# Kernel optimization log

Hardware: AMD Instinct MI355X
Metric: run time of the kernel (lower is better)

The kernel has to match this reference:

```python
import jax, jax.numpy as jnp
import numpy as np

B, N, F_IN = 2048, 64, 49   # batch of molecules, max atoms, atom feature size
D, H, L = 256, 8, 6         # conv_dim, num_heads, n_GAT_layer
DK = D // H                 # per-head dim
FC = 128                    # fc_dim
ALPHA = 0.2                 # LeakyReLU slope in GAT
NEG_INF = -1e9


def setup_inputs() -> dict:
    key = jax.random.key(0)
    ks = jax.random.split(key, 10)
    # --- padded molecular graphs ---
    n_atoms = jax.random.randint(ks[0], (B,), 16, N + 1)
    valid = jnp.arange(N)[None, :] < n_atoms[:, None]                  # [B,N]
    r = jax.random.uniform(ks[1], (B, N, N))
    adj = ((r + jnp.swapaxes(r, 1, 2)) * 0.5) < 0.08                   # symmetric sparse bonds
    adj = adj | jnp.eye(N, dtype=bool)[None]                           # self loops
    adj = adj & valid[:, :, None] & valid[:, None, :]                  # zero padded atoms
    A = adj.astype(jnp.float32)                                        # [B,N,N]
    x = jax.random.normal(ks[2], (B, N, F_IN), dtype=jnp.float32)      # [B,N,49]
    # --- parameters (xavier-like scaling) ---
    W_emb = jax.random.normal(ks[3], (D, F_IN), dtype=jnp.float32) * 0.08
    gat_W = jax.random.normal(ks[4], (L, D, D), dtype=jnp.float32) * 0.06
    gat_b = jnp.zeros((L, D), dtype=jnp.float32)
    gat_a = jax.random.normal(ks[5], (L, H, 2 * DK), dtype=jnp.float32) * 0.1
    fc_W1 = jax.random.normal(ks[6], (FC, D), dtype=jnp.float32) * 0.07
    fc_b1 = jnp.zeros((FC,), dtype=jnp.float32)
    fc_W2 = jax.random.normal(ks[7], (FC, FC), dtype=jnp.float32) * 0.09
    fc_b2 = jnp.zeros((FC,), dtype=jnp.float32)
    fc_W3 = jax.random.normal(ks[8], (1, FC), dtype=jnp.float32) * 0.09
    fc_b3 = jnp.zeros((1,), dtype=jnp.float32)
    return dict(x=x, A=A, W_emb=W_emb, gat_W=gat_W, gat_b=gat_b, gat_a=gat_a,
                fc_W1=fc_W1, fc_b1=fc_b1, fc_W2=fc_W2, fc_b2=fc_b2,
                fc_W3=fc_W3, fc_b3=fc_b3)


def _gat_layer(x, A, W, b, a):
    # x: [B,N,D], A: [B,N,N], W: [D,D], b: [D], a: [H,2*DK]
    Bm, Nn, Dd = x.shape
    h = (x @ W.T + b).reshape(Bm, Nn, H, DK)                           # [B,N,H,DK]
    a_src, a_dst = a[:, :DK], a[:, DK:]                                # [H,DK]
    e_src = jnp.einsum('bnhd,hd->bnh', h, a_src)                       # [B,N,H]
    e_dst = jnp.einsum('bnhd,hd->bnh', h, a_dst)
    e = jax.nn.leaky_relu(e_src[:, :, None, :] + e_dst[:, None, :, :], ALPHA)  # [B,Ni,Nj,H]
    e = jnp.where((A > 0)[..., None], e, NEG_INF)                      # adjacency mask
    attn = jax.nn.softmax(e, axis=2)                                   # softmax over neighbors j
    out = jnp.einsum('bijh,bjhd->bihd', attn, h).reshape(Bm, Nn, Dd)
    return jax.nn.elu(out + x)                                         # residual + ELU


def reference(x, A, W_emb, gat_W, gat_b, gat_a,
              fc_W1, fc_b1, fc_W2, fc_b2, fc_W3, fc_b3):
    h = x @ W_emb.T                                                    # embedding (no bias)
    for l in range(L):                                                 # dropout p=0 -> identity
        h = _gat_layer(h, A, gat_W[l], gat_b[l], gat_a[l])
    # masked mean readout
    node_mask = (A.sum(-1) > 0).astype(h.dtype)                        # [B,N]
    w = node_mask / node_mask.sum(-1, keepdims=True)
    g = (h * w[..., None]).sum(1)                                      # [B,D]
    # dense head: 256 -> 128 -> 128 -> 1
    z = jax.nn.relu(g @ fc_W1.T + fc_b1)
    z = jax.nn.relu(z @ fc_W2.T + fc_b2)
    z = z @ fc_W3.T + fc_b3                                            # [B,1]
    return jax.nn.elu(z).squeeze(-1) + 1.5                             # [B]
```

## Files before the change

### kernel.cpp

```cpp
#include <hip/hip_runtime.h>
#include <cstdint>
#include <cstddef>

#define B_GRAPHS 2048
#define N_NODES  64
#define FIN      49
#define D_DIM    256
#define H_HEADS  8
#define DK_DIM   32
#define L_LAYERS 6
#define ALPHA    0.2f
#define LOG2E    1.4426950408889634f

#define M_FULL     (B_GRAPHS * N_NODES)
#define WSLAB      (256 * 256)

typedef __bf16 bf16x8 __attribute__((ext_vector_type(8)));
typedef __bf16 bf16x4 __attribute__((ext_vector_type(4)));
typedef float  f32x4  __attribute__((ext_vector_type(4)));

#define MFMA16(a, b, c) __builtin_amdgcn_mfma_f32_16x16x32_bf16(a, b, c, 0, 0, 0)

__device__ __forceinline__ float leaky(float t) { return t > 0.f ? t : ALPHA * t; }

#define LDS_H     0
#define LDS_V     32768
#define LDS_E     49152
#define LDS_AM    53248
#define LDS_VALID 53760
#define LDS_TOTAL 53776

__global__ void convert_weights(const float* __restrict__ W_emb,
                                const float* __restrict__ gat_W,
                                const float* __restrict__ gat_a,
                                const float* __restrict__ gat_b,
                                __bf16* __restrict__ Wemb_b,
                                __bf16* __restrict__ Wb,
                                float* __restrict__ ba)
{
    int idx = blockIdx.x * 256 + threadIdx.x;
    if (idx < 256 * 64) {
        int n = idx >> 6, k = idx & 63;
        float f = (k < FIN) ? W_emb[n * FIN + k] : 0.f;
        Wemb_b[idx] = (__bf16)f;
    }
    if (idx < L_LAYERS * 65536) {
        Wb[idx] = (__bf16)gat_W[idx];
    }
    int o2 = idx - L_LAYERS * 65536;
    if (o2 >= 0 && o2 < L_LAYERS * 16) {
        int l = o2 >> 4, c = o2 & 15;
        int hh = c >> 1, sd = c & 1;
        const float* av = gat_a + l * 512 + hh * 64 + sd * 32;
        const float* bp = gat_b + l * 256 + hh * 32;
        float s = 0.f;
        for (int d = 0; d < 32; d++) s += av[d] * bp[d];
        ba[o2] = s;
    }
}

__global__ void convert_x(const float* __restrict__ x, __bf16* __restrict__ xb)
{
    int idx = blockIdx.x * 256 + threadIdx.x;
    int m = idx >> 6, k = idx & 63;
    xb[idx] = (__bf16)((k < FIN) ? x[m * FIN + k] : 0.f);
}

__global__ __launch_bounds__(256, 2)
void mega_gat(const float* __restrict__ A,
              const __bf16* __restrict__ xb,
              const __bf16* __restrict__ Wemb,
              const __bf16* __restrict__ Wb_all,
              const float* __restrict__ gat_b_all,
              const float* __restrict__ a_all,
              const float* __restrict__ ba_all,
              const float* __restrict__ W1, const float* __restrict__ b1,
              const float* __restrict__ W2, const float* __restrict__ b2,
              const float* __restrict__ W3, const float* __restrict__ b3,
              float* __restrict__ out)
{
    __shared__ __align__(16) char smem[LDS_TOTAL];

    const int tid  = threadIdx.x;
    const int lane = tid & 63;
    const int w    = tid >> 6;
    const int q    = lane >> 4;
    const int d15  = lane & 15;
    const int g    = blockIdx.x;

    char*  vwbase = smem + LDS_V + w * 4096;
    float* E      = (float*)(smem + LDS_E + w * 1024);
    unsigned long long* Am = (unsigned long long*)(smem + LDS_AM);

    auto h_off = [&](int i, int d) -> int {
        return i * 512 + ((((d >> 3) ^ (i & 7)) << 4)) + ((d & 7) << 1);
    };

    {
        const char* src = (const char*)(xb + (size_t)g * 4096);
        bf16x8 t0 = *(const bf16x8*)(src + tid * 16);
        bf16x8 t1 = *(const bf16x8*)(src + 4096 + tid * 16);
        int u0 = tid, u1 = 256 + tid;
        int r0 = u0 >> 3, s0 = u0 & 7;
        int r1 = u1 >> 3, s1 = u1 & 7;
        *(bf16x8*)(smem + LDS_V + r0 * 128 + ((s0 ^ (r0 & 7)) << 4)) = t0;
        *(bf16x8*)(smem + LDS_V + r1 * 128 + ((s1 ^ (r1 & 7)) << 4)) = t1;
    }
    {
        const float* Ab = A + (size_t)g * 4096;
#pragma unroll
        for (int rr = 0; rr < 16; rr++) {
            int r = w * 16 + rr;
            unsigned long long m = __ballot(Ab[r * 64 + lane] > 0.f);
            if (lane == 0) Am[r] = m;
        }
    }
    __syncthreads();

    if (w == 0) {
        unsigned long long rowm = Am[lane];
        unsigned long long vmw = __ballot((rowm >> lane) & 1ULL);
        if (lane == 0) {
            *(unsigned long long*)(smem + LDS_VALID) = vmw;
            *(float*)(smem + LDS_VALID + 8) = 1.f / (float)__popcll(vmw);
        }
    }

    {
        f32x4 acc[4][4];
#pragma unroll
        for (int i = 0; i < 4; i++)
#pragma unroll
            for (int j = 0; j < 4; j++) acc[i][j] = (f32x4){0.f, 0.f, 0.f, 0.f};
#pragma unroll
        for (int ks = 0; ks < 2; ks++) {
            const int k0 = ks * 32 + q * 8;
            const int sl = ks * 4 + q;
            bf16x8 ah[4];
#pragma unroll
            for (int mf = 0; mf < 4; mf++) {
                int r = mf * 16 + d15;
                ah[mf] = *(const bf16x8*)(smem + LDS_V + r * 128 + ((sl ^ (r & 7)) << 4));
            }
#pragma unroll
            for (int nf = 0; nf < 4; nf++) {
                bf16x8 bh = *(const bf16x8*)(Wemb + (size_t)(w * 64 + nf * 16 + d15) * 64 + k0);
#pragma unroll
                for (int mf = 0; mf < 4; mf++)
                    acc[mf][nf] = MFMA16(ah[mf], bh, acc[mf][nf]);
            }
        }
#pragma unroll
        for (int nf = 0; nf < 4; nf++) {
            int d = w * 64 + nf * 16 + d15;
#pragma unroll
            for (int mf = 0; mf < 4; mf++)
#pragma unroll
                for (int rr = 0; rr < 4; rr++) {
                    int i = mf * 16 + q * 4 + rr;
                    *(__bf16*)(smem + h_off(i, d)) = (__bf16)acc[mf][nf][rr];
                }
        }
    }
    __syncthreads();

    const unsigned long long vm = *(const unsigned long long*)(smem + LDS_VALID);

#pragma unroll 1
    for (int l = 0; l < L_LAYERS; l++) {
        const __bf16* Wl = Wb_all + (size_t)l * WSLAB;

        float a0r[2][2], a1r[2][2], bar[2][2], bvreg[4];
#pragma unroll
        for (int hp = 0; hp < 2; hp++) {
            const int head = 2 * w + hp;
#pragma unroll
            for (int sd = 0; sd < 2; sd++) {
                a0r[hp][sd] = a_all[l * 512 + head * 64 + sd * 32 + d15];
                a1r[hp][sd] = a_all[l * 512 + head * 64 + sd * 32 + 16 + d15];
                bar[hp][sd] = ba_all[l * 16 + 2 * head + sd];
            }
        }
#pragma unroll
        for (int nf = 0; nf < 4; nf++)
            bvreg[nf] = gat_b_all[l * 256 + w * 64 + nf * 16 + d15];

        f32x4 acc[4][4];
#pragma unroll
        for (int i = 0; i < 4; i++)
#pragma unroll
            for (int j = 0; j < 4; j++) acc[i][j] = (f32x4){0.f, 0.f, 0.f, 0.f};

        bf16x8 breg[3][4];
        auto loadB = [&](int buf, int ks) {
            const int k0 = ks * 32 + q * 8;
#pragma unroll
            for (int nf = 0; nf < 4; nf++)
                breg[buf][nf] = *(const bf16x8*)(Wl + (size_t)(w * 64 + nf * 16 + d15) * 256 + k0);
        };
        loadB(0, 0);
        loadB(1, 1);

#pragma unroll
        for (int ks = 0; ks < 8; ks++) {
            if (ks + 2 < 8) loadB((ks + 2) % 3, ks + 2);
            bf16x8 ah[4];
            const int sl = ks * 4 + q;
#pragma unroll
            for (int mf = 0; mf < 4; mf++) {
                int r = mf * 16 + d15;
                ah[mf] = *(const bf16x8*)(smem + r * 512 + ((sl ^ (r & 7)) << 4));
            }
#pragma unroll
            for (int nf = 0; nf < 4; nf++)
#pragma unroll
                for (int mf = 0; mf < 4; mf++)
                    acc[mf][nf] = MFMA16(ah[mf], breg[ks % 3][nf], acc[mf][nf]);
        }

        __syncthreads();

        unsigned long long msk[4];
#pragma unroll
        for (int mf = 0; mf < 4; mf++) msk[mf] = Am[mf * 16 + d15];

#pragma unroll
        for (int hl = 0; hl < 2; hl++) {
            const int head = 2 * w + hl;

#pragma unroll
            for (int sd = 0; sd < 2; sd++) {
                float a0 = a0r[hl][sd];
                float a1 = a1r[hl][sd];
                float tmp[4][4];
#pragma unroll
                for (int mf = 0; mf < 4; mf++)
#pragma unroll
                    for (int rr = 0; rr < 4; rr++)
                        tmp[mf][rr] = acc[mf][2 * hl][rr] * a0 + acc[mf][2 * hl + 1][rr] * a1;
#pragma unroll
                for (int off = 1; off <= 8; off <<= 1)
#pragma unroll
                    for (int mf = 0; mf < 4; mf++)
#pragma unroll
                        for (int rr = 0; rr < 4; rr++)
                            tmp[mf][rr] += __shfl_xor(tmp[mf][rr], off);
                float bac = bar[hl][sd];
                if (d15 == 0) {
#pragma unroll
                    for (int mf = 0; mf < 4; mf++)
#pragma unroll
                        for (int rr = 0; rr < 4; rr++)
                            E[(hl * 2 + sd) * 64 + mf * 16 + q * 4 + rr] =
                                (tmp[mf][rr] + bac) * LOG2E;
                }
            }

#pragma unroll
            for (int nfl = 0; nfl < 2; nfl++) {
                const int nf = hl * 2 + nfl;
                const int d  = nfl * 16 + d15;
                const float bv = bvreg[nf];
                char* vb = vwbase + d * 128;
#pragma unroll
                for (int mf = 0; mf < 4; mf++) {
                    int s   = mf * 2 + (q >> 1);
                    int off = ((s ^ (d & 7)) << 4) + (q & 1) * 8;
                    bf16x4 h4;
#pragma unroll
                    for (int rr = 0; rr < 4; rr++)
                        h4[rr] = (__bf16)(acc[mf][nf][rr] + bv);
                    *(bf16x4*)(vb + off) = h4;
                }
            }

            float ev = E[(hl * 2 + 1) * 64 + lane];
#pragma unroll
            for (int off = 32; off; off >>= 1) ev = fmaxf(ev, __shfl_xor(ev, off));

            float esi[4], mh[4];
#pragma unroll
            for (int mf = 0; mf < 4; mf++) {
                esi[mf] = E[(hl * 2) * 64 + mf * 16 + d15];
                mh[mf]  = leaky(esi[mf] + ev);
            }

            f32x4 pv[4][2];
#pragma unroll
            for (int mf = 0; mf < 4; mf++) {
                pv[mf][0] = (f32x4){0.f, 0.f, 0.f, 0.f};
                pv[mf][1] = (f32x4){0.f, 0.f, 0.f, 0.f};
            }
            float rs[4] = {0.f, 0.f, 0.f, 0.f};

#pragma unroll
            for (int ksj = 0; ksj < 2; ksj++) {
                const int j8 = ksj * 32 + q * 8;
                const int s  = ksj * 4 + q;
                bf16x8 vh[2];
#pragma unroll
                for (int nf2 = 0; nf2 < 2; nf2++) {
                    int d = nf2 * 16 + d15;
                    vh[nf2] = *(const bf16x8*)(vwbase + d * 128 + ((s ^ (d & 7)) << 4));
                }
                float edv[8];
#pragma unroll
                for (int e = 0; e < 8; e++) edv[e] = E[(hl * 2 + 1) * 64 + j8 + e];

#pragma unroll
                for (int mf = 0; mf < 4; mf++) {
                    unsigned int mb = (unsigned int)(msk[mf] >> j8) & 0xffu;
                    bf16x8 ph;
                    float rsum = 0.f;
#pragma unroll
                    for (int e = 0; e < 8; e++) {
                        float t = leaky(esi[mf] + edv[e]);
                        float p = ((mb >> e) & 1u)
                                    ? __builtin_amdgcn_exp2f(t - mh[mf]) : 0.f;
                        rsum += p;
                        ph[e] = (__bf16)p;
                    }
                    rs[mf] += rsum;
#pragma unroll
                    for (int nf2 = 0; nf2 < 2; nf2++)
                        pv[mf][nf2] = MFMA16(ph, vh[nf2], pv[mf][nf2]);
                }
            }

#pragma unroll
            for (int mf = 0; mf < 4; mf++) {
                float r = rs[mf];
                r += __shfl_xor(r, 16);
                r += __shfl_xor(r, 32);
                if (q == 0)
                    E[(hl * 2) * 64 + mf * 16 + d15] = (r > 0.f) ? 1.f / r : 0.f;
            }

#pragma unroll
            for (int mf = 0; mf < 4; mf++) {
#pragma unroll
                for (int nf2 = 0; nf2 < 2; nf2++) {
                    int d = head * 32 + nf2 * 16 + d15;
#pragma unroll
                    for (int rr = 0; rr < 4; rr++) {
                        int i = mf * 16 + q * 4 + rr;
                        float inv = E[(hl * 2) * 64 + i];
                        int hoff = h_off(i, d);
                        float old = (float)*(const __bf16*)(smem + hoff);
                        float o = pv[mf][nf2][rr] * inv + old;
                        o = o > 0.f ? o : __expf(o) - 1.f;
                        *(__bf16*)(smem + hoff) = (__bf16)o;
                    }
                }
            }
        }
        __syncthreads();
    }

    {
        float invc = *(const float*)(smem + LDS_VALID + 8);
        float gsum = 0.f;
#pragma unroll 8
        for (int n = 0; n < 64; n++)
            if ((vm >> n) & 1ULL)
                gsum += (float)*(const __bf16*)(smem + h_off(n, tid));

        float* gl = (float*)(smem + LDS_V);
        float* z1 = (float*)(smem + LDS_V + 1024);
        float* z2 = (float*)(smem + LDS_V + 1536);
        gl[tid] = gsum * invc;
        __syncthreads();

        if (tid < 128) {
            const float* wr = W1 + tid * 256;
            float z = 0.f;
#pragma unroll 8
            for (int k = 0; k < 256; k += 4) {
                float4 wv = *(const float4*)&wr[k];
                z += wv.x * gl[k] + wv.y * gl[k + 1] + wv.z * gl[k + 2] + wv.w * gl[k + 3];
            }
            z += b1[tid];
            z1[tid] = z > 0.f ? z : 0.f;
        }
        __syncthreads();

        if (tid < 128) {
            const float* wr = W2 + tid * 128;
            float z = 0.f;
#pragma unroll 8
            for (int k = 0; k < 128; k += 4) {
                float4 wv = *(const float4*)&wr[k];
                z += wv.x * z1[k] + wv.y * z1[k + 1] + wv.z * z1[k + 2] + wv.w * z1[k + 3];
            }
            z += b2[tid];
            z2[tid] = z > 0.f ? z : 0.f;
        }
        __syncthreads();

        if (tid < 64) {
            float p = W3[tid] * z2[tid] + W3[tid + 64] * z2[tid + 64];
#pragma unroll
            for (int off = 32; off; off >>= 1) p += __shfl_down(p, off);
            if (tid == 0) {
                float z = p + b3[0];
                out[g] = (z > 0.f ? z : __expf(z) - 1.f) + 1.5f;
            }
        }
    }
}

extern "C" void kernel_launch(void* const* d_in, const int* in_sizes, int n_in,
                              void* d_out, int out_size, void* d_ws, size_t ws_size,
                              hipStream_t stream)
{
    const float* x      = (const float*)d_in[0];
    const float* A      = (const float*)d_in[1];
    const float* W_emb  = (const float*)d_in[2];
    const float* gat_W  = (const float*)d_in[3];
    const float* gat_b  = (const float*)d_in[4];
    const float* gat_a  = (const float*)d_in[5];
    const float* fc_W1  = (const float*)d_in[6];
    const float* fc_b1  = (const float*)d_in[7];
    const float* fc_W2  = (const float*)d_in[8];
    const float* fc_b2  = (const float*)d_in[9];
    const float* fc_W3  = (const float*)d_in[10];
    const float* fc_b3  = (const float*)d_in[11];
    float* out = (float*)d_out;

    char* ws = (char*)d_ws;
    __bf16* xb     = (__bf16*)ws;
    __bf16* Wemb_b = (__bf16*)(ws + 16777216);
    __bf16* Wb     = (__bf16*)(ws + 16809984);
    float*  ba     = (float*)(ws + 17596416);

    int conv_total = L_LAYERS * 65536 + L_LAYERS * 16;
    convert_weights<<<(conv_total + 255) / 256, 256, 0, stream>>>(
        W_emb, gat_W, gat_a, gat_b, Wemb_b, Wb, ba);
    convert_x<<<M_FULL * 64 / 256, 256, 0, stream>>>(x, xb);

    mega_gat<<<B_GRAPHS, 256, 0, stream>>>(
        A, xb, Wemb_b, Wb, gat_b, gat_a, ba,
        fc_W1, fc_b1, fc_W2, fc_b2, fc_W3, fc_b3, out);
}
```

Measured before the change: 553.5 us.

## Fold attention vectors into weight matrix to compute scores via MFMA

Precomputes W^T·a_src and W^T·a_dst for each head as 16 extra rows appended to each layer's weight slab. Each wave then runs an extra 16-column MFMA tile, so the per-node attention logits come straight out of the GEMM. This replaces the per-head dot products and the 4-step cross-lane shuffle reductions. The cost is one extra MFMA N-tile per wave (5 instead of 4) plus more registers for the B buffers and accE accumulators. Rounding the folded weights to bf16 slightly changes precision.

```diff
diff --git a/kernel.cpp b/kernel.cpp
--- a/kernel.cpp
+++ b/kernel.cpp
@@ -13,7 +13,8 @@
 #define LOG2E    1.4426950408889634f
 
 #define M_FULL     (B_GRAPHS * N_NODES)
-#define WSLAB      (256 * 256)
+#define WROWS      272
+#define WSLAB      (WROWS * 256)
 
 typedef __bf16 bf16x8 __attribute__((ext_vector_type(8)));
 typedef __bf16 bf16x4 __attribute__((ext_vector_type(4)));
@@ -45,9 +46,21 @@
         Wemb_b[idx] = (__bf16)f;
     }
     if (idx < L_LAYERS * 65536) {
-        Wb[idx] = (__bf16)gat_W[idx];
-    }
-    int o2 = idx - L_LAYERS * 65536;
+        int l = idx >> 16, nk = idx & 65535;
+        Wb[l * WSLAB + nk] = (__bf16)gat_W[idx];
+    }
+    int o = idx - L_LAYERS * 65536;
+    if (o >= 0 && o < L_LAYERS * 4096) {
+        int l = o >> 12, r = o & 4095;
+        int k = r >> 4, c = r & 15;
+        int hh = c >> 1, sd = c & 1;
+        const float* av = gat_a + l * 512 + hh * 64 + sd * 32;
+        const float* wp = gat_W + ((size_t)l * 256 + hh * 32) * 256 + k;
+        float s = 0.f;
+        for (int d = 0; d < 32; d++) s += av[d] * wp[d * 256];
+        Wb[l * WSLAB + (256 + c) * 256 + k] = (__bf16)s;
+    }
+    int o2 = idx - L_LAYERS * 65536 - L_LAYERS * 4096;
     if (o2 >= 0 && o2 < L_LAYERS * 16) {
         int l = o2 >> 4, c = o2 & 15;
         int hh = c >> 1, sd = c & 1;
@@ -72,7 +85,6 @@
               const __bf16* __restrict__ Wemb,
               const __bf16* __restrict__ Wb_all,
               const float* __restrict__ gat_b_all,
-              const float* __restrict__ a_all,
               const float* __restrict__ ba_all,
               const float* __restrict__ W1, const float* __restrict__ b1,
               const float* __restrict__ W2, const float* __restrict__ b2,
@@ -170,33 +182,27 @@
     for (int l = 0; l < L_LAYERS; l++) {
         const __bf16* Wl = Wb_all + (size_t)l * WSLAB;
 
-        float a0r[2][2], a1r[2][2], bar[2][2], bvreg[4];
-#pragma unroll
-        for (int hp = 0; hp < 2; hp++) {
-            const int head = 2 * w + hp;
-#pragma unroll
-            for (int sd = 0; sd < 2; sd++) {
-                a0r[hp][sd] = a_all[l * 512 + head * 64 + sd * 32 + d15];
-                a1r[hp][sd] = a_all[l * 512 + head * 64 + sd * 32 + 16 + d15];
-                bar[hp][sd] = ba_all[l * 16 + 2 * head + sd];
-            }
-        }
+        float bvreg[4];
 #pragma unroll
         for (int nf = 0; nf < 4; nf++)
             bvreg[nf] = gat_b_all[l * 256 + w * 64 + nf * 16 + d15];
 
-        f32x4 acc[4][4];
-#pragma unroll
-        for (int i = 0; i < 4; i++)
+        f32x4 acc[4][4], accE[4];
+#pragma unroll
+        for (int i = 0; i < 4; i++) {
+            accE[i] = (f32x4){0.f, 0.f, 0.f, 0.f};
 #pragma unroll
             for (int j = 0; j < 4; j++) acc[i][j] = (f32x4){0.f, 0.f, 0.f, 0.f};
-
-        bf16x8 breg[3][4];
+        }
+
+        bf16x8 breg[3][5];
         auto loadB = [&](int buf, int ks) {
             const int k0 = ks * 32 + q * 8;
 #pragma unroll
-            for (int nf = 0; nf < 4; nf++)
-                breg[buf][nf] = *(const bf16x8*)(Wl + (size_t)(w * 64 + nf * 16 + d15) * 256 + k0);
+            for (int nt = 0; nt < 5; nt++) {
+                int n = (nt < 4) ? (w * 64 + nt * 16 + d15) : (256 + d15);
+                breg[buf][nt] = *(const bf16x8*)(Wl + (size_t)n * 256 + k0);
+            }
         };
         loadB(0, 0);
         loadB(1, 1);
@@ -212,10 +218,12 @@
                 ah[mf] = *(const bf16x8*)(smem + r * 512 + ((sl ^ (r & 7)) << 4));
             }
 #pragma unroll
-            for (int nf = 0; nf < 4; nf++)
-#pragma unroll
-                for (int mf = 0; mf < 4; mf++)
-                    acc[mf][nf] = MFMA16(ah[mf], breg[ks % 3][nf], acc[mf][nf]);
+            for (int nt = 0; nt < 5; nt++)
+#pragma unroll
+                for (int mf = 0; mf < 4; mf++) {
+                    f32x4& dst = (nt < 4) ? acc[mf][nt] : accE[mf];
+                    dst = MFMA16(ah[mf], breg[ks % 3][nt], dst);
+                }
         }
 
         __syncthreads();
@@ -223,38 +231,21 @@
         unsigned long long msk[4];
 #pragma unroll
         for (int mf = 0; mf < 4; mf++) msk[mf] = Am[mf * 16 + d15];
+
+        if (d15 >= 4 * w && d15 < 4 * w + 4) {
+            const int cl = d15 - 4 * w;
+            const float bac = ba_all[l * 16 + 4 * w + cl];
+#pragma unroll
+            for (int mf = 0; mf < 4; mf++)
+#pragma unroll
+                for (int rr = 0; rr < 4; rr++)
+                    E[cl * 64 + mf * 16 + q * 4 + rr] =
+                        (accE[mf][rr] + bac) * LOG2E;
+        }
 
 #pragma unroll
         for (int hl = 0; hl < 2; hl++) {
             const int head = 2 * w + hl;
-
-#pragma unroll
-            for (int sd = 0; sd < 2; sd++) {
-                float a0 = a0r[hl][sd];
-                float a1 = a1r[hl][sd];
-                float tmp[4][4];
-#pragma unroll
-                for (int mf = 0; mf < 4; mf++)
-#pragma unroll
-                    for (int rr = 0; rr < 4; rr++)
-                        tmp[mf][rr] = acc[mf][2 * hl][rr] * a0 + acc[mf][2 * hl + 1][rr] * a1;
-#pragma unroll
-                for (int off = 1; off <= 8; off <<= 1)
-#pragma unroll
-                    for (int mf = 0; mf < 4; mf++)
-#pragma unroll
-                        for (int rr = 0; rr < 4; rr++)
-                            tmp[mf][rr] += __shfl_xor(tmp[mf][rr], off);
-                float bac = bar[hl][sd];
-                if (d15 == 0) {
-#pragma unroll
-                    for (int mf = 0; mf < 4; mf++)
-#pragma unroll
-                        for (int rr = 0; rr < 4; rr++)
-                            E[(hl * 2 + sd) * 64 + mf * 16 + q * 4 + rr] =
-                                (tmp[mf][rr] + bac) * LOG2E;
-                }
-            }
 
 #pragma unroll
             for (int nfl = 0; nfl < 2; nfl++) {
@@ -431,14 +422,14 @@
     __bf16* xb     = (__bf16*)ws;
     __bf16* Wemb_b = (__bf16*)(ws + 16777216);
     __bf16* Wb     = (__bf16*)(ws + 16809984);
-    float*  ba     = (float*)(ws + 17596416);
-
-    int conv_total = L_LAYERS * 65536 + L_LAYERS * 16;
+    float*  ba     = (float*)(ws + 17645568);
+
+    int conv_total = L_LAYERS * 65536 + L_LAYERS * 4096 + L_LAYERS * 16;
     convert_weights<<<(conv_total + 255) / 256, 256, 0, stream>>>(
         W_emb, gat_W, gat_a, gat_b, Wemb_b, Wb, ba);
     convert_x<<<M_FULL * 64 / 256, 256, 0, stream>>>(x, xb);
 
     mega_gat<<<B_GRAPHS, 256, 0, stream>>>(
-        A, xb, Wemb_b, Wb, gat_b, gat_a, ba,
+        A, xb, Wemb_b, Wb, gat_b, ba,
         fc_W1, fc_b1, fc_W2, fc_b2, fc_W3, fc_b3, out);
 }
```

After: 599.0 us. 8.2% more time.
